# Performance work log

Hardware: AMD Instinct MI355X
Metric: run time of the kernel (lower is better)

Reference implementation:

```python
import jax, jax.numpy as jnp
import numpy as np

D = 2048       # hidden / input / output width
DEPTH = 9      # infinite_depth (layer default)


def _infinite_layer(x, inf_w, cls_w, cls_b):
    """Faithful vectorized InfiniteNeuralLayer.forward.

    Original per-(sample, j, depth) Python loops build a circulant rotation
    matrix M = cos*I + sin*(shift_down - shift_up) and apply it 3x per depth
    with angles inf_w[depth, j, 0..2]. The rotated state never depends on x,
    so we carry one state row per output index j and scan over the 27 angle
    steps, expressing M @ s as cos*s + sin*(roll(s,1) - roll(s,-1)).
    infinite_biases is unused in the original forward and is omitted.
    """
    dim = x.shape[1]
    classical = x @ cls_w + cls_b                      # [B, dim]
    # angles per j per depth step: (DEPTH, dim_j, 3) -> sequence (DEPTH*3, dim_j)
    angles = jnp.transpose(inf_w[:, :, :3], (0, 2, 1)).reshape(-1, dim)
    init = jnp.full((dim, dim), 1.0 / np.sqrt(dim), dtype=x.dtype)  # [j, state]

    def step(s, a):
        c = jnp.cos(a)[:, None]
        sn = jnp.sin(a)[:, None]
        s_new = c * s + sn * (jnp.roll(s, 1, axis=1) - jnp.roll(s, -1, axis=1))
        return s_new, None

    state, _ = jax.lax.scan(step, init, angles)        # [dim_j, dim]
    p = state[:, 0] ** 2                               # |state[0]|^2 per j
    return jnp.tanh(classical + p[None, :])            # broadcast over batch


def setup_inputs() -> dict:
    key = jax.random.key(0)
    ks = jax.random.split(key, 16)
    s = 0.02  # keep activations in sane range (original uses raw randn)
    f = jax.random.normal
    return {
        "x":      f(ks[0], (2048, D), dtype=jnp.float32),
        "w0":     f(ks[1], (D, D), dtype=jnp.float32) * s,
        "b0":     f(ks[2], (D,), dtype=jnp.float32) * s,
        "w1":     f(ks[3], (D, D), dtype=jnp.float32) * s,
        "b1":     f(ks[4], (D,), dtype=jnp.float32) * s,
        "inf_w1": f(ks[5], (DEPTH, D, D), dtype=jnp.float32),
        "cls_w1": f(ks[6], (D, D), dtype=jnp.float32) * s,
        "cls_b1": f(ks[7], (D,), dtype=jnp.float32) * s,
        "w2":     f(ks[8], (D, D), dtype=jnp.float32) * s,
        "b2":     f(ks[9], (D,), dtype=jnp.float32) * s,
        "inf_w2": f(ks[10], (DEPTH, D, D), dtype=jnp.float32),
        "cls_w2": f(ks[11], (D, D), dtype=jnp.float32) * s,
        "cls_b2": f(ks[12], (D,), dtype=jnp.float32) * s,
        "w3":     f(ks[13], (D, D), dtype=jnp.float32) * s,
        "b3":     f(ks[14], (D,), dtype=jnp.float32) * s,
    }


def reference(x, w0, b0, w1, b1, inf_w1, cls_w1, cls_b1,
              w2, b2, inf_w2, cls_w2, cls_b2, w3, b3):
    h = jax.nn.relu(x @ w0 + b0)
    h = jax.nn.relu(h @ w1 + b1)
    h = _infinite_layer(h, inf_w1, cls_w1, cls_b1)
    h = jax.nn.relu(h @ w2 + b2)
    h = _infinite_layer(h, inf_w2, cls_w2, cls_b2)
    return jax.nn.relu(h @ w3 + b3)
```

## Files before the change

kernel.cpp:

```cpp
#include <hip/hip_runtime.h>
#include <hip/hip_bf16.h>


#define DD 2048
#define DEPTH 9

#define BM 128
#define BN 64
#define BK 32
#define NT (DD / BK)

typedef __attribute__((ext_vector_type(8))) short short8;
typedef __attribute__((ext_vector_type(4))) float f32x4;

__device__ __forceinline__ unsigned short f2bf(float f) {
  unsigned u = __float_as_uint(f);
  u += 0x7FFFu + ((u >> 16) & 1u);
  return (unsigned short)(u >> 16);
}


__global__ void cvt_bf16_kernel(const float* __restrict__ s,
                                unsigned short* __restrict__ d, int n4) {
  int i = blockIdx.x * 256 + threadIdx.x;
  if (i >= n4) return;
  float4 v = reinterpret_cast<const float4*>(s)[i];
  ushort4 o;
  o.x = f2bf(v.x); o.y = f2bf(v.y); o.z = f2bf(v.z); o.w = f2bf(v.w);
  reinterpret_cast<ushort4*>(d)[i] = o;
}

__global__ void transpose2_kernel(const float* __restrict__ s0,
                                  const float* __restrict__ s1,
                                  unsigned short* __restrict__ wts) {
  __shared__ float tile[32][33];
  const float* src = blockIdx.z ? s1 : s0;
  unsigned short* dst = wts + (size_t)blockIdx.z * DD * DD;
  int bx = blockIdx.x * 32;
  int by = blockIdx.y * 32;
  int tx = threadIdx.x, ty = threadIdx.y;
#pragma unroll
  for (int i = ty; i < 32; i += 8)
    tile[i][tx] = src[(size_t)(by + i) * DD + bx + tx];
  __syncthreads();
#pragma unroll
  for (int i = ty; i < 32; i += 8)
    dst[(size_t)(bx + i) * DD + by + tx] = f2bf(tile[tx][i]);
}

__global__ void padd_kernel(const float* __restrict__ infw1,
                            const float* __restrict__ infw2,
                            const float* __restrict__ clsb1,
                            const float* __restrict__ clsb2,
                            float* __restrict__ padd1,
                            float* __restrict__ padd2) {
  int j = blockIdx.x * 256 + threadIdx.x;
  if (j >= DD) return;
  const float* inf_w = blockIdx.y ? infw2 : infw1;
  const float* cls_b = blockIdx.y ? clsb2 : clsb1;
  float* padd = blockIdx.y ? padd2 : padd1;
  float prod = 1.0f;
#pragma unroll
  for (int d = 0; d < DEPTH; ++d) {
    const float* row = inf_w + ((size_t)d * DD + j) * DD;
    prod *= cosf(row[0]) * cosf(row[1]) * cosf(row[2]);
  }
  padd[j] = cls_b[j] + prod * prod * (1.0f / (float)DD);
}


__device__ __forceinline__ void gload_lds16(const unsigned short* g,
                                            unsigned short* l) {
  __builtin_amdgcn_global_load_lds(
      (const __attribute__((address_space(1))) void*)g,
      (__attribute__((address_space(3))) void*)l, 16, 0, 0);
}

__device__ __forceinline__ void waitv6() {
  asm volatile("s_waitcnt vmcnt(6)" ::: "memory");
}
__device__ __forceinline__ void waitv3() {
  asm volatile("s_waitcnt vmcnt(3)" ::: "memory");
}
__device__ __forceinline__ void waitv0() {
  asm volatile("s_waitcnt vmcnt(0)" ::: "memory");
}
__device__ __forceinline__ void waitlgkm0() {
  asm volatile("s_waitcnt lgkmcnt(0)" ::: "memory");
}

template <int EPI>
__global__ __launch_bounds__(256) void gemm_kernel(
    const unsigned short* __restrict__ A, const unsigned short* __restrict__ Bt,
    const float* __restrict__ bias, unsigned short* __restrict__ Cb,
    float* __restrict__ Cf, const float* __restrict__ tsrc,
    unsigned short* __restrict__ tdst) {
  const int N = DD, K = DD;
  __shared__ __align__(16) unsigned char smem[36864];
  unsigned short* As = (unsigned short*)smem;
  unsigned short* Bs = (unsigned short*)(smem + 3 * BM * BK * 2);

  int tid = threadIdx.x;
  int wid = tid >> 6, lane = tid & 63;
  int wr = wid >> 1, wc = wid & 1;
  int lr = lane & 15;
  int lg = lane >> 4;

  int bid = blockIdx.x;
  int swz = (bid & 7) * 64 + (bid >> 3);
  int bcol = (swz & 31) * BN;
  int brow = (swz >> 5) * BM;

  const unsigned short* Abase = A + (size_t)brow * K;
  const unsigned short* Bbase = Bt + (size_t)bcol * K;

  auto stage = [&](int buf, int tile) {
    int kt = tile * BK;
#pragma unroll
    for (int r = 0; r < 2; ++r) {
      int chunk = r * 256 + tid;
      int row = chunk >> 2;
      int sp = chunk & 3;
      int kof = (sp ^ ((row >> 1) & 3)) * 8;
      gload_lds16(Abase + (size_t)row * K + kt + kof,
                  As + buf * (BM * BK) + (size_t)(r * 256 + wid * 64) * 8);
    }
    {
      int row = tid >> 2;
      int sp = tid & 3;
      int kof = (sp ^ ((row >> 1) & 3)) * 8;
      gload_lds16(Bbase + (size_t)row * K + kt + kof,
                  Bs + buf * (BN * BK) + (size_t)(wid * 64) * 8);
    }
  };

  f32x4 acc[4][2];
#pragma unroll
  for (int i = 0; i < 4; ++i)
#pragma unroll
    for (int j = 0; j < 2; ++j) acc[i][j] = f32x4{0.f, 0.f, 0.f, 0.f};

  auto compute = [&](int buf) {
    short8 a[4], b[2];
#pragma unroll
    for (int mt = 0; mt < 4; ++mt) {
      int row = wr * 64 + mt * 16 + lr;
      int slot = lg ^ ((row >> 1) & 3);
      a[mt] = *reinterpret_cast<const short8*>(
          &As[buf * (BM * BK) + row * BK + slot * 8]);
    }
#pragma unroll
    for (int nt = 0; nt < 2; ++nt) {
      int row = wc * 32 + nt * 16 + lr;
      int slot = lg ^ ((row >> 1) & 3);
      b[nt] = *reinterpret_cast<const short8*>(
          &Bs[buf * (BN * BK) + row * BK + slot * 8]);
    }
    __builtin_amdgcn_s_setprio(1);
#pragma unroll
    for (int mt = 0; mt < 4; ++mt)
#pragma unroll
      for (int nt = 0; nt < 2; ++nt)
        acc[mt][nt] = __builtin_amdgcn_mfma_f32_16x16x32_bf16(
            a[mt], b[nt], acc[mt][nt], 0, 0, 0);
    __builtin_amdgcn_s_setprio(0);
  };

  auto step = [&](int buf, int pf_tile, int wcase) {
    if (wcase == 0) waitv6();
    else if (wcase == 1) waitv3();
    else waitv0();
    __builtin_amdgcn_s_barrier();
    __builtin_amdgcn_sched_barrier(0);
    compute(buf);
    waitlgkm0();
    __builtin_amdgcn_s_barrier();
    __builtin_amdgcn_sched_barrier(0);
    if (pf_tile < NT) stage(buf, pf_tile);
  };

  stage(0, 0); stage(1, 1); stage(2, 2);
#pragma unroll 1
  for (int i = 0; i < 20; ++i) {
    int t = 3 * i;
    step(0, t + 3, 0);
    step(1, t + 4, 0);
    step(2, t + 5, 0);
  }
  step(0, 63, 0);
  step(1, NT, 0);
  step(2, NT, 1);
  step(0, NT, 2);

  {
    float* et = reinterpret_cast<float*>(smem);
#pragma unroll
    for (int nt = 0; nt < 2; ++nt) {
      int colb = wc * 32 + nt * 16 + lr;
      float bs = bias[bcol + colb];
#pragma unroll
      for (int mt = 0; mt < 4; ++mt) {
#pragma unroll
        for (int i = 0; i < 4; ++i) {
          int rowb = wr * 64 + mt * 16 + lg * 4 + i;
          float v = acc[mt][nt][i] + bs;
          v = (EPI == 1) ? tanhf(v) : fmaxf(v, 0.0f);
          et[rowb * 68 + colb] = v;
        }
      }
    }
    __syncthreads();
#pragma unroll
    for (int it = 0; it < 4; ++it) {
      int chunk = it * 256 + tid;
      int rowb = chunk >> 3;
      int c8 = (chunk & 7) * 8;
      float4 v0 = *reinterpret_cast<const float4*>(&et[rowb * 68 + c8]);
      float4 v1 = *reinterpret_cast<const float4*>(&et[rowb * 68 + c8 + 4]);
      size_t g = (size_t)(brow + rowb) * N + bcol + c8;
      if (EPI == 2) {
        *reinterpret_cast<float4*>(&Cf[g]) = v0;
        *reinterpret_cast<float4*>(&Cf[g + 4]) = v1;
      } else {
        uint4 o;
        o.x = (unsigned)f2bf(v0.x) | ((unsigned)f2bf(v0.y) << 16);
        o.y = (unsigned)f2bf(v0.z) | ((unsigned)f2bf(v0.w) << 16);
        o.z = (unsigned)f2bf(v1.x) | ((unsigned)f2bf(v1.y) << 16);
        o.w = (unsigned)f2bf(v1.z) | ((unsigned)f2bf(v1.w) << 16);
        *reinterpret_cast<uint4*>(&Cb[g]) = o;
      }
    }
  }

  if (tsrc != nullptr) {
    float* ft = reinterpret_cast<float*>(smem);
    __syncthreads();
#pragma unroll 1
    for (int t2 = 0; t2 < 2; ++t2) {
      int tau = bid * 2 + t2;
      int bx = (tau & 31) * 64;
      int by = (tau >> 5) * 64;
      if (t2) __syncthreads();
#pragma unroll
      for (int it = 0; it < 4; ++it) {
        int idx = it * 256 + tid;
        int r = idx >> 4, c4 = (idx & 15) * 4;
        float4 v = *reinterpret_cast<const float4*>(
            &tsrc[(size_t)(by + r) * DD + bx + c4]);
        ft[r * 65 + c4 + 0] = v.x;
        ft[r * 65 + c4 + 1] = v.y;
        ft[r * 65 + c4 + 2] = v.z;
        ft[r * 65 + c4 + 3] = v.w;
      }
      __syncthreads();
#pragma unroll
      for (int it = 0; it < 4; ++it) {
        int idx = it * 256 + tid;
        int n = idx >> 4, kq = idx & 15;
        ushort4 o;
        o.x = f2bf(ft[(kq * 4 + 0) * 65 + n]);
        o.y = f2bf(ft[(kq * 4 + 1) * 65 + n]);
        o.z = f2bf(ft[(kq * 4 + 2) * 65 + n]);
        o.w = f2bf(ft[(kq * 4 + 3) * 65 + n]);
        *reinterpret_cast<ushort4*>(&tdst[(size_t)(bx + n) * DD + by + kq * 4]) = o;
      }
    }
  }
}


extern "C" void kernel_launch(void* const* d_in, const int* in_sizes, int n_in,
                              void* d_out, int out_size, void* d_ws,
                              size_t ws_size, hipStream_t stream) {
  const float* x     = (const float*)d_in[0];
  const float* w0    = (const float*)d_in[1];
  const float* b0    = (const float*)d_in[2];
  const float* w1    = (const float*)d_in[3];
  const float* b1    = (const float*)d_in[4];
  const float* infw1 = (const float*)d_in[5];
  const float* clsw1 = (const float*)d_in[6];
  const float* clsb1 = (const float*)d_in[7];
  const float* w2    = (const float*)d_in[8];
  const float* b2    = (const float*)d_in[9];
  const float* infw2 = (const float*)d_in[10];
  const float* clsw2 = (const float*)d_in[11];
  const float* clsb2 = (const float*)d_in[12];
  const float* w3    = (const float*)d_in[13];
  const float* b3    = (const float*)d_in[14];
  float* out = (float*)d_out;

  char* ws = (char*)d_ws;
  const size_t MB = 1ull << 20;
  const size_t DDe = (size_t)DD * DD;
  unsigned short* buf0 = (unsigned short*)ws;
  unsigned short* buf1 = (unsigned short*)(ws + 8 * MB);
  unsigned short* wts  = (unsigned short*)(ws + 16 * MB);
  float* padd1 = (float*)(ws + 64 * MB);
  float* padd2 = padd1 + DD;

  transpose2_kernel<<<dim3(DD / 32, DD / 32, 2), dim3(32, 8), 0, stream>>>(
      w0, w1, wts);
  cvt_bf16_kernel<<<(int)(DDe / 4 / 256), 256, 0, stream>>>(x, buf0,
                                                            (int)(DDe / 4));
  padd_kernel<<<dim3(DD / 256, 2), 256, 0, stream>>>(infw1, infw2, clsb1,
                                                     clsb2, padd1, padd2);

  dim3 gg((DD / BM) * (DD / BN));
  gemm_kernel<0><<<gg, 256, 0, stream>>>(buf0, wts + 0 * DDe, b0,    buf1,
                                         nullptr, clsw1, wts + 2 * DDe);
  gemm_kernel<0><<<gg, 256, 0, stream>>>(buf1, wts + 1 * DDe, b1,    buf0,
                                         nullptr, w2,    wts + 3 * DDe);
  gemm_kernel<1><<<gg, 256, 0, stream>>>(buf0, wts + 2 * DDe, padd1, buf1,
                                         nullptr, clsw2, wts + 4 * DDe);
  gemm_kernel<0><<<gg, 256, 0, stream>>>(buf1, wts + 3 * DDe, b2,    buf0,
                                         nullptr, w3,    wts + 5 * DDe);
  gemm_kernel<1><<<gg, 256, 0, stream>>>(buf0, wts + 4 * DDe, padd2, buf1,
                                         nullptr, nullptr, nullptr);
  gemm_kernel<2><<<gg, 256, 0, stream>>>(buf1, wts + 5 * DDe, b3,    nullptr,
                                         out, nullptr, nullptr);
}
```

Before: 219.0 us.

## Use four LDS stages to drop per-step barrier and fuse prep kernels

The GEMM's LDS ring grows from three to four buffers, and each tile is prefetched into the slot that is not being read. This lets the second barrier and lgkmcnt wait inside every k-step be removed, halving the synchronisation per iteration. Separately, the transpose, fp32-to-bf16 conversion and padd kernels are merged into one launch, saving launch overhead. The larger LDS footprint (48KB) may lower the number of blocks per CU, and removing the barrier relies on the four-slot distance to avoid a WAR hazard between stage() and compute().

```diff
diff --git a/kernel.cpp b/kernel.cpp
--- a/kernel.cpp
+++ b/kernel.cpp
@@ -19,53 +19,52 @@
   return (unsigned short)(u >> 16);
 }
 
-
-__global__ void cvt_bf16_kernel(const float* __restrict__ s,
-                                unsigned short* __restrict__ d, int n4) {
-  int i = blockIdx.x * 256 + threadIdx.x;
-  if (i >= n4) return;
-  float4 v = reinterpret_cast<const float4*>(s)[i];
-  ushort4 o;
-  o.x = f2bf(v.x); o.y = f2bf(v.y); o.z = f2bf(v.z); o.w = f2bf(v.w);
-  reinterpret_cast<ushort4*>(d)[i] = o;
-}
-
-__global__ void transpose2_kernel(const float* __restrict__ s0,
-                                  const float* __restrict__ s1,
-                                  unsigned short* __restrict__ wts) {
-  __shared__ float tile[32][33];
-  const float* src = blockIdx.z ? s1 : s0;
-  unsigned short* dst = wts + (size_t)blockIdx.z * DD * DD;
-  int bx = blockIdx.x * 32;
-  int by = blockIdx.y * 32;
-  int tx = threadIdx.x, ty = threadIdx.y;
-#pragma unroll
-  for (int i = ty; i < 32; i += 8)
-    tile[i][tx] = src[(size_t)(by + i) * DD + bx + tx];
-  __syncthreads();
-#pragma unroll
-  for (int i = ty; i < 32; i += 8)
-    dst[(size_t)(bx + i) * DD + by + tx] = f2bf(tile[tx][i]);
-}
-
-__global__ void padd_kernel(const float* __restrict__ infw1,
-                            const float* __restrict__ infw2,
-                            const float* __restrict__ clsb1,
-                            const float* __restrict__ clsb2,
-                            float* __restrict__ padd1,
-                            float* __restrict__ padd2) {
-  int j = blockIdx.x * 256 + threadIdx.x;
-  if (j >= DD) return;
-  const float* inf_w = blockIdx.y ? infw2 : infw1;
-  const float* cls_b = blockIdx.y ? clsb2 : clsb1;
-  float* padd = blockIdx.y ? padd2 : padd1;
-  float prod = 1.0f;
-#pragma unroll
-  for (int d = 0; d < DEPTH; ++d) {
-    const float* row = inf_w + ((size_t)d * DD + j) * DD;
-    prod *= cosf(row[0]) * cosf(row[1]) * cosf(row[2]);
+__global__ __launch_bounds__(256) void prep_kernel(
+    const float* __restrict__ w0, const float* __restrict__ w1,
+    unsigned short* __restrict__ wts, const float* __restrict__ x,
+    unsigned short* __restrict__ xb, const float* __restrict__ infw1,
+    const float* __restrict__ infw2, const float* __restrict__ clsb1,
+    const float* __restrict__ clsb2, float* __restrict__ padd1,
+    float* __restrict__ padd2) {
+  int b = blockIdx.x;
+  int tid = threadIdx.x;
+  if (b < 8192) {
+    __shared__ float tile[32][33];
+    int z = b >> 12;
+    int t = b & 4095;
+    const float* src = z ? w1 : w0;
+    unsigned short* dst = wts + (size_t)z * DD * DD;
+    int bx = (t & 63) * 32;
+    int by = (t >> 6) * 32;
+    int tx = tid & 31, ty = tid >> 5;
+#pragma unroll
+    for (int i = ty; i < 32; i += 8)
+      tile[i][tx] = src[(size_t)(by + i) * DD + bx + tx];
+    __syncthreads();
+#pragma unroll
+    for (int i = ty; i < 32; i += 8)
+      dst[(size_t)(bx + i) * DD + by + tx] = f2bf(tile[tx][i]);
+  } else if (b < 12288) {
+    int i = (b - 8192) * 256 + tid;
+    float4 v = reinterpret_cast<const float4*>(x)[i];
+    ushort4 o;
+    o.x = f2bf(v.x); o.y = f2bf(v.y); o.z = f2bf(v.z); o.w = f2bf(v.w);
+    reinterpret_cast<ushort4*>(xb)[i] = o;
+  } else {
+    int jj = (b - 12288) * 256 + tid;
+    int layer = jj >> 11;
+    int j = jj & 2047;
+    const float* inf_w = layer ? infw2 : infw1;
+    const float* cls_b = layer ? clsb2 : clsb1;
+    float* padd = layer ? padd2 : padd1;
+    float prod = 1.0f;
+#pragma unroll
+    for (int d = 0; d < DEPTH; ++d) {
+      const float* row = inf_w + ((size_t)d * DD + j) * DD;
+      prod *= cosf(row[0]) * cosf(row[1]) * cosf(row[2]);
+    }
+    padd[j] = cls_b[j] + prod * prod * (1.0f / (float)DD);
   }
-  padd[j] = cls_b[j] + prod * prod * (1.0f / (float)DD);
 }
 
 
@@ -84,9 +83,6 @@
 }
 __device__ __forceinline__ void waitv0() {
   asm volatile("s_waitcnt vmcnt(0)" ::: "memory");
-}
-__device__ __forceinline__ void waitlgkm0() {
-  asm volatile("s_waitcnt lgkmcnt(0)" ::: "memory");
 }
 
 template <int EPI>
@@ -96,9 +92,9 @@
     float* __restrict__ Cf, const float* __restrict__ tsrc,
     unsigned short* __restrict__ tdst) {
   const int N = DD, K = DD;
-  __shared__ __align__(16) unsigned char smem[36864];
+  __shared__ __align__(16) unsigned char smem[49152];
   unsigned short* As = (unsigned short*)smem;
-  unsigned short* Bs = (unsigned short*)(smem + 3 * BM * BK * 2);
+  unsigned short* Bs = (unsigned short*)(smem + 4 * BM * BK * 2);
 
   int tid = threadIdx.x;
   int wid = tid >> 6, lane = tid & 63;
@@ -173,27 +169,26 @@
     __builtin_amdgcn_s_barrier();
     __builtin_amdgcn_sched_barrier(0);
     compute(buf);
-    waitlgkm0();
-    __builtin_amdgcn_s_barrier();
-    __builtin_amdgcn_sched_barrier(0);
-    if (pf_tile < NT) stage(buf, pf_tile);
+    if (pf_tile < NT) stage(pf_tile & 3, pf_tile);
   };
 
   stage(0, 0); stage(1, 1); stage(2, 2);
 #pragma unroll 1
-  for (int i = 0; i < 20; ++i) {
-    int t = 3 * i;
+  for (int i = 0; i < 15; ++i) {
+    int t = 4 * i;
     step(0, t + 3, 0);
     step(1, t + 4, 0);
     step(2, t + 5, 0);
+    step(3, t + 6, 0);
   }
   step(0, 63, 0);
   step(1, NT, 0);
   step(2, NT, 1);
-  step(0, NT, 2);
+  step(3, NT, 2);
 
   {
     float* et = reinterpret_cast<float*>(smem);
+    __syncthreads();
 #pragma unroll
     for (int nt = 0; nt < 2; ++nt) {
       int colb = wc * 32 + nt * 16 + lr;
@@ -298,12 +293,8 @@
   float* padd1 = (float*)(ws + 64 * MB);
   float* padd2 = padd1 + DD;
 
-  transpose2_kernel<<<dim3(DD / 32, DD / 32, 2), dim3(32, 8), 0, stream>>>(
-      w0, w1, wts);
-  cvt_bf16_kernel<<<(int)(DDe / 4 / 256), 256, 0, stream>>>(x, buf0,
-                                                            (int)(DDe / 4));
-  padd_kernel<<<dim3(DD / 256, 2), 256, 0, stream>>>(infw1, infw2, clsb1,
-                                                     clsb2, padd1, padd2);
+  prep_kernel<<<12304, 256, 0, stream>>>(w0, w1, wts, x, buf0, infw1, infw2,
+                                         clsb1, clsb2, padd1, padd2);
 
   dim3 gg((DD / BM) * (DD / BN));
   gemm_kernel<0><<<gg, 256, 0, stream>>>(buf0, wts + 0 * DDe, b0,    buf1,
```

After: 221.1 us. About the same (+0.9%).
